# Kernel optimization log

Measured on AMD Instinct MI355X. Metric: run time of the kernel, lower is better.

Reference implementation:

```python
import jax, jax.numpy as jnp
import numpy as np

N, CIN, COUT, V, L, SL = 16, 64, 64, 1024, 12, 3
K_LIST = [10, 20, 40]
MARKOFF = -1e20


def setup_inputs() -> dict:
    key = jax.random.key(0)
    ks = jax.random.split(key, 8)
    x = jax.random.normal(ks[0], (N, CIN, V, L), jnp.float32)
    support = jax.random.normal(ks[1], (N, SL, V, V), jnp.float32)
    s0 = 1.0 / np.sqrt(CIN)
    s1 = 1.0 / np.sqrt(4 * CIN)
    s2 = 1.0 / np.sqrt(SL * COUT + COUT)
    W0 = jax.random.normal(ks[2], (COUT, CIN), jnp.float32) * s0
    b0 = jnp.zeros((COUT,), jnp.float32)
    Ws = jax.random.normal(ks[3], (SL, COUT, 4 * CIN), jnp.float32) * s1
    bs = jnp.zeros((SL, COUT), jnp.float32)
    Wf = jax.random.normal(ks[4], (COUT, SL * COUT + COUT), jnp.float32) * s2
    bf = jnp.zeros((COUT,), jnp.float32)
    return {"x": x, "support": support, "W0": W0, "b0": b0,
            "Ws": Ws, "bs": bs, "Wf": Wf, "bf": bf}


def conv1x1(h, W, b):
    # 1x1 Conv2d over [N, C, V, L] == channel contraction
    return jnp.einsum('ncvl,oc->novl', h, W) + b[None, :, None, None]


def knn_adj(a, k):
    # batched topk along last dim; keep topk values, fill rest with -1e20
    knn_val, knn_ind = jax.lax.top_k(a, k)          # [N, V, k]
    adj = jnp.full(a.shape, MARKOFF, a.dtype)
    bi = jnp.arange(a.shape[0])[:, None, None]
    ri = jnp.arange(a.shape[1])[None, :, None]
    return adj.at[bi, ri, knn_ind].set(knn_val)


def reference(x, support, W0, b0, Ws, bs, Wf, bf):
    out = [conv1x1(x, W0, b0)]
    for i in range(SL):
        a = support[:, i]                            # [N, V, V]
        parts = []
        for k in K_LIST:
            a1 = jax.nn.softmax(knn_adj(a, min(k, V)), axis=-1)
            parts.append(jnp.einsum('ncvl,nvw->ncwl', x, a1))
        parts.append(jnp.einsum('ncvl,nvw->ncwl', x, jax.nn.softmax(a, axis=-1)))
        h = jnp.concatenate(parts, axis=1)           # [N, 4*CIN, V, L]
        out.append(conv1x1(h, Ws[i], bs[i]))
    out = jnp.concatenate(out, axis=1)               # [N, (SL+1)*COUT, V, L]
    # dropout is identity in eval mode
    return conv1x1(out, Wf, bf)
```

## Files before the change

kernel.cpp:

```cpp
#include <hip/hip_runtime.h>
#include <hip/hip_bf16.h>
#include <hip/hip_fp16.h>

#define NB 16
#define V 1024
#define LL 12
#define C64 64
#define SL 3
#define CL 768
#define KTOT 12288
#define MARKOFF -1e20f

typedef _Float16 f16x8 __attribute__((ext_vector_type(8)));
typedef __attribute__((ext_vector_type(4))) float f32x4;

static __device__ __forceinline__ unsigned short f2h(float f) {
  __half h = __float2half(f);
  return __builtin_bit_cast(unsigned short, h);
}

typedef const __attribute__((address_space(1))) unsigned int gas_u32;
typedef __attribute__((address_space(3))) unsigned int las_u32;
static __device__ __forceinline__ void gld16(const void* g, void* l) {
  __builtin_amdgcn_global_load_lds((gas_u32*)g, (las_u32*)l, 16, 0, 0);
}

static __device__ __forceinline__ unsigned long long shflx64(unsigned long long v, int m) {
  unsigned lo = __shfl_xor((unsigned)v, m);
  unsigned hi = __shfl_xor((unsigned)(v >> 32), m);
  return ((unsigned long long)hi << 32) | lo;
}
static __device__ __forceinline__ unsigned long long shfl64get(unsigned long long v, int srcLane) {
  unsigned lo = __shfl((unsigned)v, srcLane);
  unsigned hi = __shfl((unsigned)(v >> 32), srcLane);
  return ((unsigned long long)hi << 32) | lo;
}
static __device__ __forceinline__ float k2f(unsigned kk) {
  unsigned u = (kk & 0x80000000u) ? (kk & 0x7FFFFFFFu) : ~kk;
  return __uint_as_float(u);
}

__global__ __launch_bounds__(256) void k_prep(const float* __restrict__ W0,
                                              const float* __restrict__ b0,
                                              const float* __restrict__ Ws,
                                              const float* __restrict__ bs,
                                              const float* __restrict__ Wf,
                                              const float* __restrict__ bf,
                                              float* __restrict__ D,
                                              float* __restrict__ cb,
                                              unsigned short* __restrict__ Gt) {
  int b = blockIdx.x;
  int t = threadIdx.x;
  int o = t >> 2, cp = t & 3;
  if (b < 12) {
    int i = b >> 2, g = b & 3;
    for (int c = cp * 16; c < cp * 16 + 16; c++) {
      float acc = 0.f;
      for (int c2 = 0; c2 < 64; c2++)
        acc += Wf[o * 256 + 64 * (i + 1) + c2] * Ws[i * 16384 + c2 * 256 + g * 64 + c];
      Gt[(size_t)(b * 64 + o) * 64 + c] = f2h(acc);
    }
  } else {
    for (int c = cp * 16; c < cp * 16 + 16; c++) {
      float acc = 0.f;
      for (int c2 = 0; c2 < 64; c2++)
        acc += Wf[o * 256 + c2] * W0[c2 * 64 + c];
      D[o * 64 + c] = acc;
    }
    if (t < 64) {
      float acc = bf[t];
      for (int c2 = 0; c2 < 64; c2++) acc += Wf[t * 256 + c2] * b0[c2];
      for (int i = 0; i < 3; i++)
        for (int c2 = 0; c2 < 64; c2++) acc += Wf[t * 256 + 64 * (i + 1) + c2] * bs[i * 64 + c2];
      cb[t] = acc;
    }
  }
}

__global__ __launch_bounds__(256) void k_stats(const float* __restrict__ support,
                                               float* __restrict__ stats) {
  int t = threadIdx.x;
  int lane = t & 63, wid = t >> 6;
  int row = blockIdx.x * 4 + wid;
  const float* a = support + (size_t)row * 1024;

  __shared__ unsigned long long cand[4][128];

  float va[16];
  const float4* a4 = (const float4*)a;
#pragma unroll
  for (int j = 0; j < 4; j++) {
    float4 f = a4[lane + 64 * j];
    va[j * 4 + 0] = f.x; va[j * 4 + 1] = f.y; va[j * 4 + 2] = f.z; va[j * 4 + 3] = f.w;
  }

  float m = va[0];
#pragma unroll
  for (int q = 1; q < 16; q++) m = fmaxf(m, va[q]);
#pragma unroll
  for (int off = 32; off; off >>= 1) m = fmaxf(m, __shfl_xor(m, off));

  float zf = 0.f;
#pragma unroll
  for (int q = 0; q < 16; q++) zf += __expf(va[q] - m);
#pragma unroll
  for (int off = 32; off; off >>= 1) zf += __shfl_xor(zf, off);

  unsigned ky[16];
#pragma unroll
  for (int q = 0; q < 16; q++) {
    unsigned u = __float_as_uint(va[q]);
    ky[q] = (u & 0x80000000u) ? ~u : (u | 0x80000000u);
  }

  unsigned Klo = 0u, Khi = 0xFFFFFFFFu;
  unsigned K = 0xBFB33333u;
  int c = 0;
  bool ok = false;
  for (int it = 0; it < 40; ++it) {
    int cl = 0;
#pragma unroll
    for (int q = 0; q < 16; q++) cl += (ky[q] > K) ? 1 : 0;
    c = cl;
#pragma unroll
    for (int off = 32; off; off >>= 1) c += __shfl_xor(c, off);
    if (c >= 40 && c <= 128) { ok = true; break; }
    if (c > 128) Klo = K; else Khi = K;
    if (Khi - Klo <= 1u) break;
    K = Klo + ((Khi - Klo) >> 1);
  }
  bool special = !ok;
  if (special) {
    K = Khi;
    int cl = 0;
#pragma unroll
    for (int q = 0; q < 16; q++) cl += (ky[q] > K) ? 1 : 0;
    c = cl;
#pragma unroll
    for (int off = 32; off; off >>= 1) c += __shfl_xor(c, off);
  }

  int cl = 0;
#pragma unroll
  for (int q = 0; q < 16; q++) cl += (ky[q] > K) ? 1 : 0;
  int pre = cl;
#pragma unroll
  for (int off = 1; off < 64; off <<= 1) {
    int t2 = __shfl_up(pre, off);
    if (lane >= off) pre += t2;
  }
  int o = pre - cl;
  cand[wid][lane] = 0ull;
  cand[wid][64 + lane] = 0ull;
  __syncthreads();
#pragma unroll
  for (int q = 0; q < 16; q++) {
    if (ky[q] > K) {
      unsigned idx = (unsigned)(lane * 4 + (q >> 2) * 256 + (q & 3));
      cand[wid][o++] = ((unsigned long long)ky[q] << 32) | (unsigned)(~idx);
    }
  }
  __syncthreads();
  unsigned long long s0 = cand[wid][lane];
  unsigned long long s1 = cand[wid][64 + lane];

#pragma unroll
  for (int k2 = 2; k2 <= 128; k2 <<= 1) {
#pragma unroll
    for (int j = k2 >> 1; j > 0; j >>= 1) {
      if (j == 64) {
        unsigned long long mx = (s0 > s1) ? s0 : s1;
        unsigned long long mn = (s0 > s1) ? s1 : s0;
        s0 = mx; s1 = mn;
      } else {
        bool lower = ((lane & j) == 0);
        bool d0 = ((lane & k2) == 0);
        bool d1 = (((64 + lane) & k2) == 0);
        unsigned long long q0 = shflx64(s0, j);
        unsigned long long q1 = shflx64(s1, j);
        bool kmax0 = (lower == d0);
        bool kmax1 = (lower == d1);
        s0 = (kmax0 == (s0 > q0)) ? s0 : q0;
        s1 = (kmax1 == (s1 > q1)) ? s1 : q1;
      }
    }
  }

  int nval = (c < 40) ? c : 40;
  float pv = 0.f;
  if (lane < nval) pv = __expf(k2f((unsigned)(s0 >> 32)) - m);
  float z10 = (lane < 10) ? pv : 0.f;
  float z20 = (lane < 20) ? pv : 0.f;
  float z40 = pv;
#pragma unroll
  for (int off = 32; off; off >>= 1) {
    z10 += __shfl_xor(z10, off);
    z20 += __shfl_xor(z20, off);
    z40 += __shfl_xor(z40, off);
  }

  float T[3], wcut[3], iZ[3];
  const int kk3[3] = {10, 20, 40};
#pragma unroll
  for (int s3 = 0; s3 < 3; s3++) {
    int k = kk3[s3];
    if (!special || k <= c) {
      unsigned long long sk = shfl64get(s0, k - 1);
      T[s3] = k2f((unsigned)(sk >> 32));
      wcut[s3] = (float)(~(unsigned)sk);
      float Zk = (s3 == 0) ? z10 : ((s3 == 1) ? z20 : z40);
      iZ[s3] = 1.f / Zk;
    } else {
      int r = k - c;
      float vt = k2f(K);
      T[s3] = vt;
      int lo2 = -1, hi2 = 1023;
      while (hi2 - lo2 > 1) {
        int mid = (lo2 + hi2) >> 1;
        int cnt = 0;
#pragma unroll
        for (int q = 0; q < 16; q++) {
          int idx = lane * 4 + (q >> 2) * 256 + (q & 3);
          cnt += (ky[q] == K && idx <= mid) ? 1 : 0;
        }
#pragma unroll
        for (int off = 32; off; off >>= 1) cnt += __shfl_xor(cnt, off);
        if (cnt >= r) hi2 = mid; else lo2 = mid;
      }
      wcut[s3] = (float)hi2;
      iZ[s3] = 1.f / (z40 + (float)r * __expf(vt - m));
    }
  }

  if (lane == 0) {
    float* sp = stats + (size_t)row * 12;
    float4 w0v = {m, 1.f / zf, T[0], T[1]};
    float4 w1v = {T[2], iZ[0], iZ[1], iZ[2]};
    float4 w2v = {wcut[0], wcut[1], wcut[2], 0.f};
    *(float4*)(sp + 0) = w0v;
    *(float4*)(sp + 4) = w1v;
    *(float4*)(sp + 8) = w2v;
  }
}

__global__ __launch_bounds__(256) void k_init(const float* __restrict__ x,
                                              const float* __restrict__ D,
                                              const float* __restrict__ cb,
                                              float* __restrict__ out) {
  int b = blockIdx.x;
  int n = b >> 10, w = b & 1023;
  int t = threadIdx.x;
  __shared__ float xs[768];
  __shared__ float Ds[64 * 65];
  __shared__ float cbs[64];
  const float* xb = x + (size_t)n * 786432 + w * 12;
  for (int u = t; u < 768; u += 256) {
    int c = u / 12, l2 = u - c * 12;
    xs[u] = xb[(size_t)c * 12288 + l2];
  }
  for (int u = t; u < 4096; u += 256) Ds[(u >> 6) * 65 + (u & 63)] = D[u];
  if (t < 64) cbs[t] = cb[t];
  __syncthreads();
  float* ob = out + (size_t)n * 786432 + w * 12;
  for (int u = t; u < 768; u += 256) {
    int o = u / 12, l2 = u - o * 12;
    float accv = cbs[o];
    const float* dr = &Ds[o * 65];
#pragma unroll
    for (int c = 0; c < 64; c++) accv += dr[c] * xs[c * 12 + l2];
    ob[(size_t)o * 12288 + l2] = accv;
  }
}

__global__ __launch_bounds__(256) void k_ybuild(const float* __restrict__ x,
                                                const unsigned short* __restrict__ Gt,
                                                unsigned short* __restrict__ Y,
                                                int s) {
  int b = blockIdx.x;
  int nc = b / 576;
  int rem2 = b - nc * 576;
  int mt = rem2 / 6, nt = rem2 - (rem2 / 6) * 6;
  int n = s + nc;
  int l = mt >> 3;
  int v0 = (mt & 7) << 7;

  __shared__ __align__(16) char smem[34816];
  unsigned short(*A2)[128][32] = (unsigned short(*)[128][32])smem;
  unsigned short(*B2)[128][32] = (unsigned short(*)[128][32])(smem + 16384);
  unsigned short(*R)[136] = (unsigned short(*)[136])smem;

  int t = threadIdx.x;
  int lane = t & 63, wid = t >> 6;
  int wm = (wid >> 1) * 64, wn = (wid & 1) * 64;

  {
    int mloc = t >> 1, half = t & 1;
    const float* xp = x + (size_t)n * 786432 + (size_t)(half * 32) * 12288 + (size_t)(v0 + mloc) * 12 + l;
#pragma unroll
    for (int sg = 0; sg < 4; sg++) {
      unsigned q0 = f2h(xp[(size_t)(sg * 8 + 0) * 12288]) | ((unsigned)f2h(xp[(size_t)(sg * 8 + 1) * 12288]) << 16);
      unsigned q1 = f2h(xp[(size_t)(sg * 8 + 2) * 12288]) | ((unsigned)f2h(xp[(size_t)(sg * 8 + 3) * 12288]) << 16);
      unsigned q2 = f2h(xp[(size_t)(sg * 8 + 4) * 12288]) | ((unsigned)f2h(xp[(size_t)(sg * 8 + 5) * 12288]) << 16);
      unsigned q3 = f2h(xp[(size_t)(sg * 8 + 6) * 12288]) | ((unsigned)f2h(xp[(size_t)(sg * 8 + 7) * 12288]) << 16);
      uint4 q = {q0, q1, q2, q3};
      *(uint4*)&A2[half][mloc][sg * 8] = q;
    }
  }
  {
    int row = t >> 1, half = t & 1;
    const unsigned short* gp = Gt + (size_t)(nt * 128 + row) * 64 + half * 32;
#pragma unroll
    for (int sg = 0; sg < 4; sg++)
      *(uint4*)&B2[half][row][sg * 8] = *(const uint4*)(gp + sg * 8);
  }
  __syncthreads();

  f32x4 acc[4][4];
#pragma unroll
  for (int fm = 0; fm < 4; fm++)
#pragma unroll
    for (int fn = 0; fn < 4; fn++) acc[fm][fn] = (f32x4){0.f, 0.f, 0.f, 0.f};

  int ko = (lane >> 4) * 8;
#pragma unroll
  for (int half = 0; half < 2; half++) {
    f16x8 af[4], bfr[4];
#pragma unroll
    for (int fm = 0; fm < 4; fm++) af[fm] = *(const f16x8*)&A2[half][wm + fm * 16 + (lane & 15)][ko];
#pragma unroll
    for (int fn = 0; fn < 4; fn++) bfr[fn] = *(const f16x8*)&B2[half][wn + fn * 16 + (lane & 15)][ko];
#pragma unroll
    for (int fm = 0; fm < 4; fm++)
#pragma unroll
      for (int fn = 0; fn < 4; fn++)
        acc[fm][fn] = __builtin_amdgcn_mfma_f32_16x16x32_f16(af[fm], bfr[fn], acc[fm][fn], 0, 0, 0);
  }
  __syncthreads();

#pragma unroll
  for (int fm = 0; fm < 4; fm++)
#pragma unroll
    for (int fn = 0; fn < 4; fn++) {
      int col = wn + fn * 16 + (lane & 15);
      int mrow = wm + fm * 16 + (lane >> 4) * 4;
      unsigned lo = (unsigned)f2h(acc[fm][fn][0]) | ((unsigned)f2h(acc[fm][fn][1]) << 16);
      unsigned hi = (unsigned)f2h(acc[fm][fn][2]) | ((unsigned)f2h(acc[fm][fn][3]) << 16);
      uint2 pk = {lo, hi};
      *(uint2*)&R[col][mrow] = pk;
    }
  __syncthreads();

  {
    int row = t >> 1, hseg = t & 1;
    int ncol = nt * 128 + row;
    int ig = ncol >> 6, o = ncol & 63;
    size_t gbase = ((size_t)nc * 768 + (size_t)(o * 12 + l)) * 12288 + (size_t)ig * 1024 + v0 + hseg * 64;
#pragma unroll
    for (int sg = 0; sg < 8; sg++)
      *(uint4*)(Y + gbase + sg * 8) = *(const uint4*)&R[row][hseg * 64 + sg * 8];
  }
}

__global__ __launch_bounds__(256) void k_buildA(const float* __restrict__ support,
                                                const float* __restrict__ stats,
                                                unsigned short* __restrict__ Abuf,
                                                int s) {
  int b = blockIdx.x;
  int nc = b / 3072;
  int rem2 = b - nc * 3072;
  int i = rem2 >> 10;
  int tile = rem2 & 1023;
  int v0 = (tile >> 5) << 5;
  int w0 = (tile & 31) << 5;
  int n = s + nc;
  const float* sup = support + (size_t)(n * 3 + i) * 1024 * 1024;
  const float* stb = stats + (size_t)(n * 3 + i) * 1024 * 12;

  __shared__ float S[32][33];
  __shared__ float st[32][12];
  int t = threadIdx.x;
  {
    int vl = t >> 3, wseg = t & 7;
    const float* p = sup + (size_t)(v0 + vl) * 1024 + w0 + wseg * 4;
    float4 f = *(const float4*)p;
    S[vl][wseg * 4 + 0] = f.x;
    S[vl][wseg * 4 + 1] = f.y;
    S[vl][wseg * 4 + 2] = f.z;
    S[vl][wseg * 4 + 3] = f.w;
  }
  for (int u = t; u < 384; u += 256) {
    int vl = u / 12, q = u - vl * 12;
    st[vl][q] = stb[(size_t)(v0 + vl) * 12 + q];
  }
  __syncthreads();

  int w_loc = t >> 3, vseg = t & 7;
  float wg = (float)(w0 + w_loc);
  unsigned short bv[4][4];
#pragma unroll
  for (int j = 0; j < 4; j++) {
    int vl = vseg * 4 + j;
    float aa = S[vl][w_loc];
    float m = st[vl][0], izf = st[vl][1];
    float T10 = st[vl][2], T20 = st[vl][3], T40 = st[vl][4];
    float iz10 = st[vl][5], iz20 = st[vl][6], iz40 = st[vl][7];
    float w10 = st[vl][8], w20 = st[vl][9], w40 = st[vl][10];
    float ee = __expf(aa - m);
    bool in10 = (aa > T10) || (aa == T10 && wg <= w10);
    bool in20 = (aa > T20) || (aa == T20 && wg <= w20);
    bool in40 = (aa > T40) || (aa == T40 && wg <= w40);
    bv[3][j] = f2h(ee * izf);
    bv[2][j] = f2h(in40 ? ee * iz40 : 0.f);
    bv[1][j] = f2h(in20 ? ee * iz20 : 0.f);
    bv[0][j] = f2h(in10 ? ee * iz10 : 0.f);
  }
  size_t base = ((size_t)nc * 1024 + w0 + w_loc) * 12288 + (size_t)i * 4096 + v0 + vseg * 4;
#pragma unroll
  for (int g = 0; g < 4; g++) {
    uint2 pk;
    pk.x = (unsigned)bv[g][0] | ((unsigned)bv[g][1] << 16);
    pk.y = (unsigned)bv[g][2] | ((unsigned)bv[g][3] << 16);
    *(uint2*)(Abuf + base + (size_t)g * 1024) = pk;
  }
}

__global__ __launch_bounds__(256) void k_biggemm(const unsigned short* __restrict__ A,
                                                 const unsigned short* __restrict__ Y,
                                                 float* __restrict__ out,
                                                 int s) {
  int b = blockIdx.x;
  int cpx = gridDim.x >> 3;
  b = (b & 7) * cpx + (b >> 3);

  int nc = b / 48;
  int rem2 = b - nc * 48;
  int mt = rem2 / 6, nt = rem2 - (rem2 / 6) * 6;
  int n = s + nc;

  __shared__ __align__(16) unsigned short A3[128][32];
  __shared__ __align__(16) unsigned short B3[128][32];

  int t = threadIdx.x;
  int lane = t & 63, wid = t >> 6;
  int wm = (wid >> 1) * 64, wn = (wid & 1) * 64;

  const unsigned short* Ab = A + (size_t)nc * 12582912 + (size_t)(mt * 128) * 12288;
  const unsigned short* Yb = Y + (size_t)nc * 9437184 + (size_t)(nt * 128) * 12288;

  int srow = t >> 2;
  int scol = (t & 3) * 8;
  const unsigned short* gA0 = Ab + (size_t)srow * 12288 + scol;
  const unsigned short* gA1 = gA0 + (size_t)64 * 12288;
  const unsigned short* gB0 = Yb + (size_t)srow * 12288 + scol;
  const unsigned short* gB1 = gB0 + (size_t)64 * 12288;
  unsigned short* lA0 = &A3[0][0] + (size_t)t * 8;
  unsigned short* lA1 = lA0 + 2048;
  unsigned short* lB0 = &B3[0][0] + (size_t)t * 8;
  unsigned short* lB1 = lB0 + 2048;

  f32x4 acc[4][4];
#pragma unroll
  for (int fm = 0; fm < 4; fm++)
#pragma unroll
    for (int fn = 0; fn < 4; fn++) acc[fm][fn] = (f32x4){0.f, 0.f, 0.f, 0.f};

  int ko = (lane >> 4) * 8;

  for (int kt = 0; kt < 384; kt++) {
    __syncthreads();
    gld16(gA0, lA0);
    gld16(gA1, lA1);
    gld16(gB0, lB0);
    gld16(gB1, lB1);
    gA0 += 32; gA1 += 32; gB0 += 32; gB1 += 32;
    __syncthreads();
    f16x8 af[4], bfr[4];
#pragma unroll
    for (int fm = 0; fm < 4; fm++) af[fm] = *(const f16x8*)&A3[wm + fm * 16 + (lane & 15)][ko];
#pragma unroll
    for (int fn = 0; fn < 4; fn++) bfr[fn] = *(const f16x8*)&B3[wn + fn * 16 + (lane & 15)][ko];
#pragma unroll
    for (int fm = 0; fm < 4; fm++)
#pragma unroll
      for (int fn = 0; fn < 4; fn++)
        acc[fm][fn] = __builtin_amdgcn_mfma_f32_16x16x32_f16(af[fm], bfr[fn], acc[fm][fn], 0, 0, 0);
  }

  float* ob = out + (size_t)n * 786432;
#pragma unroll
  for (int fn = 0; fn < 4; fn++) {
    int col = nt * 128 + wn + fn * 16 + (lane & 15);
    int oo = col / 12;
    int ll2 = col - oo * 12;
    float* cbase = ob + (size_t)oo * 12288 + ll2;
#pragma unroll
    for (int fm = 0; fm < 4; fm++) {
      int w = mt * 128 + wm + fm * 16 + (lane >> 4) * 4;
      float* p = cbase + (size_t)w * 12;
#pragma unroll
      for (int r = 0; r < 4; r++) p[r * 12] += acc[fm][fn][r];
    }
  }
}

extern "C" void kernel_launch(void* const* d_in, const int* in_sizes, int n_in,
                              void* d_out, int out_size, void* d_ws, size_t ws_size,
                              hipStream_t stream) {
  const float* x = (const float*)d_in[0];
  const float* support = (const float*)d_in[1];
  const float* W0 = (const float*)d_in[2];
  const float* b0 = (const float*)d_in[3];
  const float* Ws = (const float*)d_in[4];
  const float* bs = (const float*)d_in[5];
  const float* Wf = (const float*)d_in[6];
  const float* bf = (const float*)d_in[7];
  float* out = (float*)d_out;
  char* ws = (char*)d_ws;

  float* stats = (float*)ws;
  float* D = (float*)(ws + 2359296);
  float* cb = (float*)(ws + 2375680);
  unsigned short* Gt = (unsigned short*)(ws + 2375936);
  const size_t fixed_end = 2474240;
  const size_t szY = 18874368;
  const size_t szA = 25165824;

  int C = 1;
  if (ws_size > fixed_end) {
    size_t remb = ws_size - fixed_end;
    size_t c = remb / (szY + szA);
    if (c > 16) c = 16;
    if (c < 1) c = 1;
    C = (int)c;
  }
  unsigned short* Ybuf = (unsigned short*)(ws + fixed_end);
  unsigned short* Abuf = (unsigned short*)(ws + fixed_end + (size_t)C * szY);

  k_prep<<<13, 256, 0, stream>>>(W0, b0, Ws, bs, Wf, bf, D, cb, Gt);
  k_stats<<<12288, 256, 0, stream>>>(support, stats);
  k_init<<<16384, 256, 0, stream>>>(x, D, cb, out);
  for (int s = 0; s < 16; s += C) {
    int Cc = (16 - s) < C ? (16 - s) : C;
    k_ybuild<<<Cc * 576, 256, 0, stream>>>(x, Gt, Ybuf, s);
    k_buildA<<<Cc * 3072, 256, 0, stream>>>(support, stats, Abuf, s);
    k_biggemm<<<Cc * 48, 256, 0, stream>>>(Abuf, Ybuf, out, s);
  }
}
```

Baseline: 1.179 ms.

## Double-buffer LDS tiles and swizzle layout in big GEMM kernel

The big GEMM main loop now uses two LDS buffers, so the next K-tile is fetched with global_load_lds while MFMAs run on the current one. This removes one of the two barriers per iteration. Global source columns are also permuted by an XOR-like rotation based on row, and the fragment read offsets are adjusted to match, which is meant to cut LDS bank conflicts on the 16-byte fragment reads. It doubles LDS use per block, which may lower occupancy. It also assumes the single barrier per iteration is enough to order the async LDS loads.

```diff
diff --git a/kernel.cpp b/kernel.cpp
--- a/kernel.cpp
+++ b/kernel.cpp
@@ -437,8 +437,7 @@
   int mt = rem2 / 6, nt = rem2 - (rem2 / 6) * 6;
   int n = s + nc;
 
-  __shared__ __align__(16) unsigned short A3[128][32];
-  __shared__ __align__(16) unsigned short B3[128][32];
+  __shared__ __align__(16) unsigned short SM[2][2][4096];
 
   int t = threadIdx.x;
   int lane = t & 63, wid = t >> 6;
@@ -447,16 +446,13 @@
   const unsigned short* Ab = A + (size_t)nc * 12582912 + (size_t)(mt * 128) * 12288;
   const unsigned short* Yb = Y + (size_t)nc * 9437184 + (size_t)(nt * 128) * 12288;
 
-  int srow = t >> 2;
-  int scol = (t & 3) * 8;
-  const unsigned short* gA0 = Ab + (size_t)srow * 12288 + scol;
-  const unsigned short* gA1 = gA0 + (size_t)64 * 12288;
-  const unsigned short* gB0 = Yb + (size_t)srow * 12288 + scol;
-  const unsigned short* gB1 = gB0 + (size_t)64 * 12288;
-  unsigned short* lA0 = &A3[0][0] + (size_t)t * 8;
-  unsigned short* lA1 = lA0 + 2048;
-  unsigned short* lB0 = &B3[0][0] + (size_t)t * 8;
-  unsigned short* lB1 = lB0 + 2048;
+  int d0 = t, d1 = t + 256;
+  int r0 = d0 >> 2, c0 = ((d0 & 3) - ((r0 >> 1) & 3)) & 3;
+  int r1 = d1 >> 2, c1 = ((d1 & 3) - ((r1 >> 1) & 3)) & 3;
+  const unsigned short* gA0 = Ab + (size_t)r0 * 12288 + c0 * 8;
+  const unsigned short* gA1 = Ab + (size_t)r1 * 12288 + c1 * 8;
+  const unsigned short* gB0 = Yb + (size_t)r0 * 12288 + c0 * 8;
+  const unsigned short* gB1 = Yb + (size_t)r1 * 12288 + c1 * 8;
 
   f32x4 acc[4][4];
 #pragma unroll
@@ -464,26 +460,42 @@
 #pragma unroll
     for (int fn = 0; fn < 4; fn++) acc[fm][fn] = (f32x4){0.f, 0.f, 0.f, 0.f};
 
-  int ko = (lane >> 4) * 8;
-
+  int mrow = lane & 15;
+  int cprime = ((((lane >> 4) + ((lane >> 1) & 3)) & 3)) * 8;
+
+  gld16(gA0, &SM[0][0][d0 * 8]);
+  gld16(gA1, &SM[0][0][d1 * 8]);
+  gld16(gB0, &SM[0][1][d0 * 8]);
+  gld16(gB1, &SM[0][1][d1 * 8]);
+  gA0 += 32; gA1 += 32; gB0 += 32; gB1 += 32;
+  __syncthreads();
+
+  int cur = 0;
   for (int kt = 0; kt < 384; kt++) {
-    __syncthreads();
-    gld16(gA0, lA0);
-    gld16(gA1, lA1);
-    gld16(gB0, lB0);
-    gld16(gB1, lB1);
-    gA0 += 32; gA1 += 32; gB0 += 32; gB1 += 32;
-    __syncthreads();
+    if (kt < 383) {
+      int nb = cur ^ 1;
+      gld16(gA0, &SM[nb][0][d0 * 8]);
+      gld16(gA1, &SM[nb][0][d1 * 8]);
+      gld16(gB0, &SM[nb][1][d0 * 8]);
+      gld16(gB1, &SM[nb][1][d1 * 8]);
+      gA0 += 32; gA1 += 32; gB0 += 32; gB1 += 32;
+    }
+    const unsigned short* At = &SM[cur][0][0];
+    const unsigned short* Bt = &SM[cur][1][0];
     f16x8 af[4], bfr[4];
 #pragma unroll
-    for (int fm = 0; fm < 4; fm++) af[fm] = *(const f16x8*)&A3[wm + fm * 16 + (lane & 15)][ko];
-#pragma unroll
-    for (int fn = 0; fn < 4; fn++) bfr[fn] = *(const f16x8*)&B3[wn + fn * 16 + (lane & 15)][ko];
+    for (int fm = 0; fm < 4; fm++)
+      af[fm] = *(const f16x8*)(At + (wm + fm * 16 + mrow) * 32 + cprime);
+#pragma unroll
+    for (int fn = 0; fn < 4; fn++)
+      bfr[fn] = *(const f16x8*)(Bt + (wn + fn * 16 + mrow) * 32 + cprime);
 #pragma unroll
     for (int fm = 0; fm < 4; fm++)
 #pragma unroll
       for (int fn = 0; fn < 4; fn++)
         acc[fm][fn] = __builtin_amdgcn_mfma_f32_16x16x32_f16(af[fm], bfr[fn], acc[fm][fn], 0, 0, 0);
+    __syncthreads();
+    cur ^= 1;
   }
 
   float* ob = out + (size_t)n * 786432;
```

Result: slower. 1.207 ms (+2.3%).

## Triple-buffer big GEMM LDS loads and reuse x tile across N-tiles in ybuild

Applied to the files above, without the earlier changes.

The main GEMM now uses a three-slot LDS ring with asynchronous global-to-LDS loads issued two tiles ahead. Explicit vmcnt waits and a single barrier per k-step replace the two syncthreads per iteration, so memory latency can overlap MFMA work. The Y-build kernel loads and converts each x tile once, keeps its fragments in registers, and loops over all six output column tiles. This cuts redundant x reads and conversions at the cost of fewer, longer blocks and triple the LDS per GEMM block.

```diff
diff --git a/kernel.cpp b/kernel.cpp
--- a/kernel.cpp
+++ b/kernel.cpp
@@ -277,21 +277,22 @@
                                                 unsigned short* __restrict__ Y,
                                                 int s) {
   int b = blockIdx.x;
-  int nc = b / 576;
-  int rem2 = b - nc * 576;
-  int mt = rem2 / 6, nt = rem2 - (rem2 / 6) * 6;
+  int nc = b / 96;
+  int mt = b - nc * 96;
   int n = s + nc;
   int l = mt >> 3;
   int v0 = (mt & 7) << 7;
 
   __shared__ __align__(16) char smem[34816];
-  unsigned short(*A2)[128][32] = (unsigned short(*)[128][32])smem;
-  unsigned short(*B2)[128][32] = (unsigned short(*)[128][32])(smem + 16384);
+  unsigned short* A2 = (unsigned short*)smem;
+  unsigned short* B2 = (unsigned short*)smem;
   unsigned short(*R)[136] = (unsigned short(*)[136])smem;
 
   int t = threadIdx.x;
   int lane = t & 63, wid = t >> 6;
   int wm = (wid >> 1) * 64, wn = (wid & 1) * 64;
+  int ko = (lane >> 4) * 8;
+  int mrow = lane & 15;
 
   {
     int mloc = t >> 1, half = t & 1;
@@ -303,61 +304,76 @@
       unsigned q2 = f2h(xp[(size_t)(sg * 8 + 4) * 12288]) | ((unsigned)f2h(xp[(size_t)(sg * 8 + 5) * 12288]) << 16);
       unsigned q3 = f2h(xp[(size_t)(sg * 8 + 6) * 12288]) | ((unsigned)f2h(xp[(size_t)(sg * 8 + 7) * 12288]) << 16);
       uint4 q = {q0, q1, q2, q3};
-      *(uint4*)&A2[half][mloc][sg * 8] = q;
-    }
-  }
-  {
-    int row = t >> 1, half = t & 1;
-    const unsigned short* gp = Gt + (size_t)(nt * 128 + row) * 64 + half * 32;
-#pragma unroll
-    for (int sg = 0; sg < 4; sg++)
-      *(uint4*)&B2[half][row][sg * 8] = *(const uint4*)(gp + sg * 8);
+      *(uint4*)&A2[(size_t)half * 4096 + (size_t)mloc * 32 + sg * 8] = q;
+    }
   }
   __syncthreads();
 
-  f32x4 acc[4][4];
-#pragma unroll
-  for (int fm = 0; fm < 4; fm++)
-#pragma unroll
-    for (int fn = 0; fn < 4; fn++) acc[fm][fn] = (f32x4){0.f, 0.f, 0.f, 0.f};
-
-  int ko = (lane >> 4) * 8;
-#pragma unroll
-  for (int half = 0; half < 2; half++) {
-    f16x8 af[4], bfr[4];
-#pragma unroll
-    for (int fm = 0; fm < 4; fm++) af[fm] = *(const f16x8*)&A2[half][wm + fm * 16 + (lane & 15)][ko];
-#pragma unroll
-    for (int fn = 0; fn < 4; fn++) bfr[fn] = *(const f16x8*)&B2[half][wn + fn * 16 + (lane & 15)][ko];
+  f16x8 af[2][4];
+#pragma unroll
+  for (int half = 0; half < 2; half++)
 #pragma unroll
     for (int fm = 0; fm < 4; fm++)
+      af[half][fm] = *(const f16x8*)(A2 + half * 4096 + (wm + fm * 16 + mrow) * 32 + ko);
+  __syncthreads();
+
+  const unsigned short* gG[4];
+#pragma unroll
+  for (int i = 0; i < 4; i++) {
+    int d = t + 256 * i;
+    int half = d >> 9, row = (d >> 2) & 127, sg = d & 3;
+    gG[i] = Gt + (size_t)row * 64 + half * 32 + sg * 8;
+  }
+
+  for (int nt = 0; nt < 6; nt++) {
+#pragma unroll
+    for (int i = 0; i < 4; i++)
+      gld16(gG[i] + (size_t)nt * 8192, smem + ((size_t)t + 256 * i) * 16);
+    __syncthreads();
+
+    f32x4 acc[4][4];
+#pragma unroll
+    for (int fm = 0; fm < 4; fm++)
+#pragma unroll
+      for (int fn = 0; fn < 4; fn++) acc[fm][fn] = (f32x4){0.f, 0.f, 0.f, 0.f};
+
+#pragma unroll
+    for (int half = 0; half < 2; half++) {
+      f16x8 bfr[4];
 #pragma unroll
       for (int fn = 0; fn < 4; fn++)
-        acc[fm][fn] = __builtin_amdgcn_mfma_f32_16x16x32_f16(af[fm], bfr[fn], acc[fm][fn], 0, 0, 0);
-  }
-  __syncthreads();
-
-#pragma unroll
-  for (int fm = 0; fm < 4; fm++)
-#pragma unroll
-    for (int fn = 0; fn < 4; fn++) {
-      int col = wn + fn * 16 + (lane & 15);
-      int mrow = wm + fm * 16 + (lane >> 4) * 4;
-      unsigned lo = (unsigned)f2h(acc[fm][fn][0]) | ((unsigned)f2h(acc[fm][fn][1]) << 16);
-      unsigned hi = (unsigned)f2h(acc[fm][fn][2]) | ((unsigned)f2h(acc[fm][fn][3]) << 16);
-      uint2 pk = {lo, hi};
-      *(uint2*)&R[col][mrow] = pk;
-    }
-  __syncthreads();
-
-  {
-    int row = t >> 1, hseg = t & 1;
-    int ncol = nt * 128 + row;
-    int ig = ncol >> 6, o = ncol & 63;
-    size_t gbase = ((size_t)nc * 768 + (size_t)(o * 12 + l)) * 12288 + (size_t)ig * 1024 + v0 + hseg * 64;
-#pragma unroll
-    for (int sg = 0; sg < 8; sg++)
-      *(uint4*)(Y + gbase + sg * 8) = *(const uint4*)&R[row][hseg * 64 + sg * 8];
+        bfr[fn] = *(const f16x8*)(B2 + half * 4096 + (wn + fn * 16 + mrow) * 32 + ko);
+#pragma unroll
+      for (int fm = 0; fm < 4; fm++)
+#pragma unroll
+        for (int fn = 0; fn < 4; fn++)
+          acc[fm][fn] = __builtin_amdgcn_mfma_f32_16x16x32_f16(af[half][fm], bfr[fn], acc[fm][fn], 0, 0, 0);
+    }
+    __syncthreads();
+
+#pragma unroll
+    for (int fm = 0; fm < 4; fm++)
+#pragma unroll
+      for (int fn = 0; fn < 4; fn++) {
+        int col = wn + fn * 16 + mrow;
+        int mr = wm + fm * 16 + (lane >> 4) * 4;
+        unsigned lo = (unsigned)f2h(acc[fm][fn][0]) | ((unsigned)f2h(acc[fm][fn][1]) << 16);
+        unsigned hi = (unsigned)f2h(acc[fm][fn][2]) | ((unsigned)f2h(acc[fm][fn][3]) << 16);
+        uint2 pk = {lo, hi};
+        *(uint2*)&R[col][mr] = pk;
+      }
+    __syncthreads();
+
+    {
+      int row = t >> 1, hseg = t & 1;
+      int ncol = nt * 128 + row;
+      int ig = ncol >> 6, o = ncol & 63;
+      size_t gbase = ((size_t)nc * 768 + (size_t)(o * 12 + l)) * 12288 + (size_t)ig * 1024 + v0 + hseg * 64;
+#pragma unroll
+      for (int sg = 0; sg < 8; sg++)
+        *(uint4*)(Y + gbase + sg * 8) = *(const uint4*)&R[row][hseg * 64 + sg * 8];
+    }
+    __syncthreads();
   }
 }
 
@@ -437,8 +453,8 @@
   int mt = rem2 / 6, nt = rem2 - (rem2 / 6) * 6;
   int n = s + nc;
 
-  __shared__ __align__(16) unsigned short A3[128][32];
-  __shared__ __align__(16) unsigned short B3[128][32];
+  __shared__ __align__(16) unsigned short SA[3][4096];
+  __shared__ __align__(16) unsigned short SB[3][4096];
 
   int t = threadIdx.x;
   int lane = t & 63, wid = t >> 6;
@@ -453,10 +469,6 @@
   const unsigned short* gA1 = gA0 + (size_t)64 * 12288;
   const unsigned short* gB0 = Yb + (size_t)srow * 12288 + scol;
   const unsigned short* gB1 = gB0 + (size_t)64 * 12288;
-  unsigned short* lA0 = &A3[0][0] + (size_t)t * 8;
-  unsigned short* lA1 = lA0 + 2048;
-  unsigned short* lB0 = &B3[0][0] + (size_t)t * 8;
-  unsigned short* lB1 = lB0 + 2048;
 
   f32x4 acc[4][4];
 #pragma unroll
@@ -465,26 +477,68 @@
     for (int fn = 0; fn < 4; fn++) acc[fm][fn] = (f32x4){0.f, 0.f, 0.f, 0.f};
 
   int ko = (lane >> 4) * 8;
-
-  for (int kt = 0; kt < 384; kt++) {
-    __syncthreads();
-    gld16(gA0, lA0);
-    gld16(gA1, lA1);
-    gld16(gB0, lB0);
-    gld16(gB1, lB1);
-    gA0 += 32; gA1 += 32; gB0 += 32; gB1 += 32;
-    __syncthreads();
-    f16x8 af[4], bfr[4];
-#pragma unroll
-    for (int fm = 0; fm < 4; fm++) af[fm] = *(const f16x8*)&A3[wm + fm * 16 + (lane & 15)][ko];
-#pragma unroll
-    for (int fn = 0; fn < 4; fn++) bfr[fn] = *(const f16x8*)&B3[wn + fn * 16 + (lane & 15)][ko];
-#pragma unroll
-    for (int fm = 0; fm < 4; fm++)
-#pragma unroll
-      for (int fn = 0; fn < 4; fn++)
-        acc[fm][fn] = __builtin_amdgcn_mfma_f32_16x16x32_f16(af[fm], bfr[fn], acc[fm][fn], 0, 0, 0);
-  }
+  int mrow = lane & 15;
+
+#define ISSUE_TILE(J)                                   \
+  do {                                                  \
+    unsigned short* lA = &SA[(J)][0] + (size_t)t * 8;   \
+    unsigned short* lB = &SB[(J)][0] + (size_t)t * 8;   \
+    gld16(gA0, lA);                                     \
+    gld16(gA1, lA + 2048);                              \
+    gld16(gB0, lB);                                     \
+    gld16(gB1, lB + 2048);                              \
+    gA0 += 32; gA1 += 32; gB0 += 32; gB1 += 32;         \
+  } while (0)
+
+#define COMPUTE_TILE(J)                                                          \
+  do {                                                                           \
+    const unsigned short* At = &SA[(J)][0];                                      \
+    const unsigned short* Bt = &SB[(J)][0];                                      \
+    f16x8 af[4], bfr[4];                                                         \
+    _Pragma("unroll")                                                            \
+    for (int fm = 0; fm < 4; fm++)                                               \
+      af[fm] = *(const f16x8*)(At + (wm + fm * 16 + mrow) * 32 + ko);            \
+    _Pragma("unroll")                                                            \
+    for (int fn = 0; fn < 4; fn++)                                               \
+      bfr[fn] = *(const f16x8*)(Bt + (wn + fn * 16 + mrow) * 32 + ko);           \
+    _Pragma("unroll")                                                            \
+    for (int fm = 0; fm < 4; fm++)                                               \
+      _Pragma("unroll")                                                          \
+      for (int fn = 0; fn < 4; fn++)                                             \
+        acc[fm][fn] = __builtin_amdgcn_mfma_f32_16x16x32_f16(af[fm], bfr[fn],    \
+                                                             acc[fm][fn], 0, 0, 0); \
+  } while (0)
+
+  ISSUE_TILE(0);
+  ISSUE_TILE(1);
+  __builtin_amdgcn_sched_barrier(0);
+  asm volatile("s_waitcnt vmcnt(4)");
+  __builtin_amdgcn_sched_barrier(0);
+  __builtin_amdgcn_s_barrier();
+  __builtin_amdgcn_sched_barrier(0);
+
+  int j = 0;
+  for (int kt = 0; kt < 382; kt++) {
+    int jn = j + 2; if (jn >= 3) jn -= 3;
+    ISSUE_TILE(jn);
+    COMPUTE_TILE(j);
+    __builtin_amdgcn_sched_barrier(0);
+    asm volatile("s_waitcnt vmcnt(4)");
+    __builtin_amdgcn_sched_barrier(0);
+    __builtin_amdgcn_s_barrier();
+    __builtin_amdgcn_sched_barrier(0);
+    j = (j == 2) ? 0 : j + 1;
+  }
+  COMPUTE_TILE(1);
+  __builtin_amdgcn_sched_barrier(0);
+  asm volatile("s_waitcnt vmcnt(0)");
+  __builtin_amdgcn_sched_barrier(0);
+  __builtin_amdgcn_s_barrier();
+  __builtin_amdgcn_sched_barrier(0);
+  COMPUTE_TILE(2);
+
+#undef ISSUE_TILE
+#undef COMPUTE_TILE
 
   float* ob = out + (size_t)n * 786432;
 #pragma unroll
@@ -541,7 +595,7 @@
   k_init<<<16384, 256, 0, stream>>>(x, D, cb, out);
   for (int s = 0; s < 16; s += C) {
     int Cc = (16 - s) < C ? (16 - s) : C;
-    k_ybuild<<<Cc * 576, 256, 0, stream>>>(x, Gt, Ybuf, s);
+    k_ybuild<<<Cc * 96, 256, 0, stream>>>(x, Gt, Ybuf, s);
     k_buildA<<<Cc * 3072, 256, 0, stream>>>(support, stats, Abuf, s);
     k_biggemm<<<Cc * 48, 256, 0, stream>>>(Abuf, Ybuf, out, s);
   }
```

Result: no change. 1.181 ms (+0.2%).

## Widen GEMM K-tile with swizzled LDS and loop ybuild over column tiles

Applied to the files above, without the earlier changes.

The big GEMM now stages 64-wide K tiles per iteration instead of 32, using an XOR-style rotated LDS layout to avoid bank conflicts, which halves the number of barrier pairs in the main loop. The Y-building kernel now converts and loads the x tile once per block and loops over all six Gt column tiles via direct-to-LDS loads, rather than launching a block per column tile and reloading and reconverting x each time. This cuts redundant global reads and conversions but doubles LDS use in the GEMM and makes ybuild blocks longer and serial, with fewer blocks in flight.

```diff
diff --git a/kernel.cpp b/kernel.cpp
--- a/kernel.cpp
+++ b/kernel.cpp
@@ -277,21 +277,22 @@
                                                 unsigned short* __restrict__ Y,
                                                 int s) {
   int b = blockIdx.x;
-  int nc = b / 576;
-  int rem2 = b - nc * 576;
-  int mt = rem2 / 6, nt = rem2 - (rem2 / 6) * 6;
+  int nc = b / 96;
+  int mt = b - nc * 96;
   int n = s + nc;
   int l = mt >> 3;
   int v0 = (mt & 7) << 7;
 
   __shared__ __align__(16) char smem[34816];
-  unsigned short(*A2)[128][32] = (unsigned short(*)[128][32])smem;
-  unsigned short(*B2)[128][32] = (unsigned short(*)[128][32])(smem + 16384);
+  unsigned short* A2 = (unsigned short*)smem;
+  unsigned short* B2 = (unsigned short*)smem;
   unsigned short(*R)[136] = (unsigned short(*)[136])smem;
 
   int t = threadIdx.x;
   int lane = t & 63, wid = t >> 6;
   int wm = (wid >> 1) * 64, wn = (wid & 1) * 64;
+  int ko = (lane >> 4) * 8;
+  int mrow = lane & 15;
 
   {
     int mloc = t >> 1, half = t & 1;
@@ -303,61 +304,76 @@
       unsigned q2 = f2h(xp[(size_t)(sg * 8 + 4) * 12288]) | ((unsigned)f2h(xp[(size_t)(sg * 8 + 5) * 12288]) << 16);
       unsigned q3 = f2h(xp[(size_t)(sg * 8 + 6) * 12288]) | ((unsigned)f2h(xp[(size_t)(sg * 8 + 7) * 12288]) << 16);
       uint4 q = {q0, q1, q2, q3};
-      *(uint4*)&A2[half][mloc][sg * 8] = q;
-    }
-  }
-  {
-    int row = t >> 1, half = t & 1;
-    const unsigned short* gp = Gt + (size_t)(nt * 128 + row) * 64 + half * 32;
-#pragma unroll
-    for (int sg = 0; sg < 4; sg++)
-      *(uint4*)&B2[half][row][sg * 8] = *(const uint4*)(gp + sg * 8);
+      *(uint4*)&A2[(size_t)half * 4096 + (size_t)mloc * 32 + sg * 8] = q;
+    }
   }
   __syncthreads();
 
-  f32x4 acc[4][4];
-#pragma unroll
-  for (int fm = 0; fm < 4; fm++)
-#pragma unroll
-    for (int fn = 0; fn < 4; fn++) acc[fm][fn] = (f32x4){0.f, 0.f, 0.f, 0.f};
-
-  int ko = (lane >> 4) * 8;
-#pragma unroll
-  for (int half = 0; half < 2; half++) {
-    f16x8 af[4], bfr[4];
-#pragma unroll
-    for (int fm = 0; fm < 4; fm++) af[fm] = *(const f16x8*)&A2[half][wm + fm * 16 + (lane & 15)][ko];
-#pragma unroll
-    for (int fn = 0; fn < 4; fn++) bfr[fn] = *(const f16x8*)&B2[half][wn + fn * 16 + (lane & 15)][ko];
+  f16x8 af[2][4];
+#pragma unroll
+  for (int half = 0; half < 2; half++)
 #pragma unroll
     for (int fm = 0; fm < 4; fm++)
+      af[half][fm] = *(const f16x8*)(A2 + half * 4096 + (wm + fm * 16 + mrow) * 32 + ko);
+  __syncthreads();
+
+  const unsigned short* gG[4];
+#pragma unroll
+  for (int i = 0; i < 4; i++) {
+    int d = t + 256 * i;
+    int half = d >> 9, row = (d >> 2) & 127, sg = d & 3;
+    gG[i] = Gt + (size_t)row * 64 + half * 32 + sg * 8;
+  }
+
+  for (int nt = 0; nt < 6; nt++) {
+#pragma unroll
+    for (int i = 0; i < 4; i++)
+      gld16(gG[i] + (size_t)nt * 8192, smem + ((size_t)t + 256 * i) * 16);
+    __syncthreads();
+
+    f32x4 acc[4][4];
+#pragma unroll
+    for (int fm = 0; fm < 4; fm++)
+#pragma unroll
+      for (int fn = 0; fn < 4; fn++) acc[fm][fn] = (f32x4){0.f, 0.f, 0.f, 0.f};
+
+#pragma unroll
+    for (int half = 0; half < 2; half++) {
+      f16x8 bfr[4];
 #pragma unroll
       for (int fn = 0; fn < 4; fn++)
-        acc[fm][fn] = __builtin_amdgcn_mfma_f32_16x16x32_f16(af[fm], bfr[fn], acc[fm][fn], 0, 0, 0);
-  }
-  __syncthreads();
-
-#pragma unroll
-  for (int fm = 0; fm < 4; fm++)
-#pragma unroll
-    for (int fn = 0; fn < 4; fn++) {
-      int col = wn + fn * 16 + (lane & 15);
-      int mrow = wm + fm * 16 + (lane >> 4) * 4;
-      unsigned lo = (unsigned)f2h(acc[fm][fn][0]) | ((unsigned)f2h(acc[fm][fn][1]) << 16);
-      unsigned hi = (unsigned)f2h(acc[fm][fn][2]) | ((unsigned)f2h(acc[fm][fn][3]) << 16);
-      uint2 pk = {lo, hi};
-      *(uint2*)&R[col][mrow] = pk;
-    }
-  __syncthreads();
-
-  {
-    int row = t >> 1, hseg = t & 1;
-    int ncol = nt * 128 + row;
-    int ig = ncol >> 6, o = ncol & 63;
-    size_t gbase = ((size_t)nc * 768 + (size_t)(o * 12 + l)) * 12288 + (size_t)ig * 1024 + v0 + hseg * 64;
-#pragma unroll
-    for (int sg = 0; sg < 8; sg++)
-      *(uint4*)(Y + gbase + sg * 8) = *(const uint4*)&R[row][hseg * 64 + sg * 8];
+        bfr[fn] = *(const f16x8*)(B2 + half * 4096 + (wn + fn * 16 + mrow) * 32 + ko);
+#pragma unroll
+      for (int fm = 0; fm < 4; fm++)
+#pragma unroll
+        for (int fn = 0; fn < 4; fn++)
+          acc[fm][fn] = __builtin_amdgcn_mfma_f32_16x16x32_f16(af[half][fm], bfr[fn], acc[fm][fn], 0, 0, 0);
+    }
+    __syncthreads();
+
+#pragma unroll
+    for (int fm = 0; fm < 4; fm++)
+#pragma unroll
+      for (int fn = 0; fn < 4; fn++) {
+        int col = wn + fn * 16 + mrow;
+        int mr = wm + fm * 16 + (lane >> 4) * 4;
+        unsigned lo = (unsigned)f2h(acc[fm][fn][0]) | ((unsigned)f2h(acc[fm][fn][1]) << 16);
+        unsigned hi = (unsigned)f2h(acc[fm][fn][2]) | ((unsigned)f2h(acc[fm][fn][3]) << 16);
+        uint2 pk = {lo, hi};
+        *(uint2*)&R[col][mr] = pk;
+      }
+    __syncthreads();
+
+    {
+      int row = t >> 1, hseg = t & 1;
+      int ncol = nt * 128 + row;
+      int ig = ncol >> 6, o = ncol & 63;
+      size_t gbase = ((size_t)nc * 768 + (size_t)(o * 12 + l)) * 12288 + (size_t)ig * 1024 + v0 + hseg * 64;
+#pragma unroll
+      for (int sg = 0; sg < 8; sg++)
+        *(uint4*)(Y + gbase + sg * 8) = *(const uint4*)&R[row][hseg * 64 + sg * 8];
+    }
+    __syncthreads();
   }
 }
 
@@ -437,8 +453,8 @@
   int mt = rem2 / 6, nt = rem2 - (rem2 / 6) * 6;
   int n = s + nc;
 
-  __shared__ __align__(16) unsigned short A3[128][32];
-  __shared__ __align__(16) unsigned short B3[128][32];
+  __shared__ __align__(16) unsigned short SA[128 * 64];
+  __shared__ __align__(16) unsigned short SB[128 * 64];
 
   int t = threadIdx.x;
   int lane = t & 63, wid = t >> 6;
@@ -447,16 +463,16 @@
   const unsigned short* Ab = A + (size_t)nc * 12582912 + (size_t)(mt * 128) * 12288;
   const unsigned short* Yb = Y + (size_t)nc * 9437184 + (size_t)(nt * 128) * 12288;
 
-  int srow = t >> 2;
-  int scol = (t & 3) * 8;
-  const unsigned short* gA0 = Ab + (size_t)srow * 12288 + scol;
-  const unsigned short* gA1 = gA0 + (size_t)64 * 12288;
-  const unsigned short* gB0 = Yb + (size_t)srow * 12288 + scol;
-  const unsigned short* gB1 = gB0 + (size_t)64 * 12288;
-  unsigned short* lA0 = &A3[0][0] + (size_t)t * 8;
-  unsigned short* lA1 = lA0 + 2048;
-  unsigned short* lB0 = &B3[0][0] + (size_t)t * 8;
-  unsigned short* lB1 = lB0 + 2048;
+  const unsigned short* gA[4];
+  const unsigned short* gB[4];
+#pragma unroll
+  for (int i = 0; i < 4; i++) {
+    int d = t + 256 * i;
+    int row = d >> 3, dcol = d & 7;
+    int c = (dcol - (row & 7)) & 7;
+    gA[i] = Ab + (size_t)row * 12288 + c * 8;
+    gB[i] = Yb + (size_t)row * 12288 + c * 8;
+  }
 
   f32x4 acc[4][4];
 #pragma unroll
@@ -464,26 +480,36 @@
 #pragma unroll
     for (int fn = 0; fn < 4; fn++) acc[fm][fn] = (f32x4){0.f, 0.f, 0.f, 0.f};
 
-  int ko = (lane >> 4) * 8;
-
-  for (int kt = 0; kt < 384; kt++) {
+  int mrow = lane & 15;
+  int cp0 = ((((lane >> 4) + (lane & 7)) & 7)) * 8;
+  int cp1 = ((((lane >> 4) + 4 + (lane & 7)) & 7)) * 8;
+
+  for (int kt = 0; kt < 192; kt++) {
     __syncthreads();
-    gld16(gA0, lA0);
-    gld16(gA1, lA1);
-    gld16(gB0, lB0);
-    gld16(gB1, lB1);
-    gA0 += 32; gA1 += 32; gB0 += 32; gB1 += 32;
+#pragma unroll
+    for (int i = 0; i < 4; i++) {
+      gld16(gA[i], (char*)SA + ((size_t)t + 256 * i) * 16);
+      gld16(gB[i], (char*)SB + ((size_t)t + 256 * i) * 16);
+      gA[i] += 64;
+      gB[i] += 64;
+    }
     __syncthreads();
-    f16x8 af[4], bfr[4];
-#pragma unroll
-    for (int fm = 0; fm < 4; fm++) af[fm] = *(const f16x8*)&A3[wm + fm * 16 + (lane & 15)][ko];
-#pragma unroll
-    for (int fn = 0; fn < 4; fn++) bfr[fn] = *(const f16x8*)&B3[wn + fn * 16 + (lane & 15)][ko];
-#pragma unroll
-    for (int fm = 0; fm < 4; fm++)
+#pragma unroll
+    for (int ks = 0; ks < 2; ks++) {
+      int cpo = ks ? cp1 : cp0;
+      f16x8 af[4], bfr[4];
+#pragma unroll
+      for (int fm = 0; fm < 4; fm++)
+        af[fm] = *(const f16x8*)&SA[(wm + fm * 16 + mrow) * 64 + cpo];
 #pragma unroll
       for (int fn = 0; fn < 4; fn++)
-        acc[fm][fn] = __builtin_amdgcn_mfma_f32_16x16x32_f16(af[fm], bfr[fn], acc[fm][fn], 0, 0, 0);
+        bfr[fn] = *(const f16x8*)&SB[(wn + fn * 16 + mrow) * 64 + cpo];
+#pragma unroll
+      for (int fm = 0; fm < 4; fm++)
+#pragma unroll
+        for (int fn = 0; fn < 4; fn++)
+          acc[fm][fn] = __builtin_amdgcn_mfma_f32_16x16x32_f16(af[fm], bfr[fn], acc[fm][fn], 0, 0, 0);
+    }
   }
 
   float* ob = out + (size_t)n * 786432;
@@ -541,7 +567,7 @@
   k_init<<<16384, 256, 0, stream>>>(x, D, cb, out);
   for (int s = 0; s < 16; s += C) {
     int Cc = (16 - s) < C ? (16 - s) : C;
-    k_ybuild<<<Cc * 576, 256, 0, stream>>>(x, Gt, Ybuf, s);
+    k_ybuild<<<Cc * 96, 256, 0, stream>>>(x, Gt, Ybuf, s);
     k_buildA<<<Cc * 3072, 256, 0, stream>>>(support, stats, Abuf, s);
     k_biggemm<<<Cc * 48, 256, 0, stream>>>(Abuf, Ybuf, out, s);
   }
```

After: 1.284 ms. 8.8% more time.
